# Kernel optimization log

Measured on AMD Instinct MI355X. Metric: run time of the kernel, lower is better.

## Reference

```python
import jax, jax.numpy as jnp
import numpy as np

EMBED_DIM = 1024
NUM_HEADS = 16
HEAD_DIM = EMBED_DIM // NUM_HEADS
KERNEL = 3
PAD = KERNEL // 2
B, L = 4, 1024


def conv1d(x, w, b):
    # x: [B, D, L], w: [D_out, D_in, K], b: [D_out]; 'same' padding like nn.Conv1d(padding=K//2)
    y = jax.lax.conv_general_dilated(
        x, w, window_strides=(1,), padding=[(PAD, PAD)],
        dimension_numbers=('NCH', 'OIH', 'NCH'))
    return y + b[None, :, None]


def setup_inputs() -> dict:
    key = jax.random.key(0)
    ks = jax.random.split(key, 12)
    fan = EMBED_DIM * KERNEL
    bound = 1.0 / np.sqrt(fan)
    def wconv(k):
        return jax.random.uniform(k, (EMBED_DIM, EMBED_DIM, KERNEL), jnp.float32, -bound, bound)
    def bconv(k):
        return jax.random.uniform(k, (EMBED_DIM,), jnp.float32, -bound, bound)
    return {
        'query': jax.random.normal(ks[0], (B, L, EMBED_DIM), jnp.float32),
        'key': jax.random.normal(ks[1], (B, L, EMBED_DIM), jnp.float32),
        'value': jax.random.normal(ks[2], (B, L, EMBED_DIM), jnp.float32),
        'key_padding_mask': jax.random.randint(ks[3], (B, L), 0, 2) > 0,
        'attn_mask': jnp.zeros((L, L), jnp.float32),
        'q_w': wconv(ks[4]), 'q_b': bconv(ks[5]),
        'k_w': wconv(ks[6]), 'k_b': bconv(ks[7]),
        'v_w': wconv(ks[8]), 'v_b': bconv(ks[9]),
        'o_w': wconv(ks[10]), 'o_b': bconv(ks[11]),
    }


def reference(query, key, value, key_padding_mask, attn_mask,
              q_w, q_b, k_w, k_b, v_w, v_b, o_w, o_b):
    scale = HEAD_DIM ** -0.5
    # projections: [B, D, L]
    q = conv1d(jnp.swapaxes(query, 1, 2), q_w, q_b)
    k = conv1d(jnp.swapaxes(key, 1, 2), k_w, k_b)
    v = conv1d(jnp.swapaxes(value, 1, 2), v_w, v_b)
    # [B, H, d, L]
    q = q.reshape(B, NUM_HEADS, HEAD_DIM, L)
    k = k.reshape(B, NUM_HEADS, HEAD_DIM, L)
    v = v.reshape(B, NUM_HEADS, HEAD_DIM, L)
    # scores: [B, H, L, L]
    scores = jnp.einsum('bhdi,bhdj->bhij', q, k) * scale
    scores = scores + attn_mask[None, None, :, :]
    scores = jnp.where(key_padding_mask[:, None, None, :], -jnp.inf, scores)
    attn = jax.nn.softmax(scores, axis=-1)  # dropout p=0 (eval) -> identity
    out = jnp.einsum('bhij,bhdj->bhdi', attn, v)  # [B, H, d, L]
    out = out.reshape(B, EMBED_DIM, L)
    out = conv1d(out, o_w, o_b)
    return jnp.swapaxes(out, 1, 2)  # [B, L, D]
```

## Files before the change

kernel.cpp:

```cpp
#include <hip/hip_runtime.h>
#include <math.h>

#define NB 4
#define NL 1024
#define ND 1024
#define NH 16
#define HD 64
#define PLN 4194304

typedef __attribute__((ext_vector_type(8))) short bf16x8;
typedef __attribute__((ext_vector_type(4))) float f32x4;

static __device__ __forceinline__ unsigned short f32_to_bf16(float f) {
  unsigned u = __float_as_uint(f);
  u += 0x7FFFu + ((u >> 16) & 1u);
  return (unsigned short)(u >> 16);
}
static __device__ __forceinline__ float bf16_to_f32(unsigned short s) {
  return __uint_as_float(((unsigned)s) << 16);
}
static __device__ __forceinline__ float exp2_f(float x) {
  float r;
  asm("v_exp_f32 %0, %1" : "=v"(r) : "v"(x));
  return r;
}

static __device__ __forceinline__ void split8(float4 a, float4 b, bf16x8* hi, bf16x8* lo) {
  unsigned u[8] = {__float_as_uint(a.x), __float_as_uint(a.y),
                   __float_as_uint(a.z), __float_as_uint(a.w),
                   __float_as_uint(b.x), __float_as_uint(b.y),
                   __float_as_uint(b.z), __float_as_uint(b.w)};
  union { unsigned p[4]; bf16x8 v; } H, L;
#pragma unroll
  for (int p = 0; p < 4; ++p) {
    unsigned u0 = u[2 * p], u1 = u[2 * p + 1];
    H.p[p] = __builtin_amdgcn_perm(u1, u0, 0x07060302u);
    unsigned l0 = __float_as_uint(__uint_as_float(u0) - __uint_as_float(u0 & 0xFFFF0000u));
    unsigned l1 = __float_as_uint(__uint_as_float(u1) - __uint_as_float(u1 & 0xFFFF0000u));
    L.p[p] = __builtin_amdgcn_perm(l1, l0, 0x07060302u);
  }
  *hi = H.v; *lo = L.v;
}

__global__ __launch_bounds__(256) void wcvt_kernel(
    const float* __restrict__ w0, const float* __restrict__ w1,
    const float* __restrict__ w2, const float* __restrict__ w3,
    unsigned short* __restrict__ wb, int* __restrict__ flag)
{
  if (blockIdx.x == 0 && blockIdx.y == 0 && threadIdx.x == 0) flag[0] = 0;
  const int t = blockIdx.y;
  const int o = blockIdx.x;
  const float* w = (t == 0) ? w0 : (t == 1) ? w1 : (t == 2) ? w2 : w3;
  unsigned short* hi = wb + (size_t)t * 6 * (1u << 20);
  unsigned short* lo = hi + 3 * (1u << 20);
  const int tid = threadIdx.x;
  float v[12];
  const float* src = w + (size_t)o * (ND * 3) + tid * 12;
#pragma unroll
  for (int j = 0; j < 3; ++j) {
    float4 f = *(const float4*)(src + j * 4);
    v[j * 4 + 0] = f.x; v[j * 4 + 1] = f.y; v[j * 4 + 2] = f.z; v[j * 4 + 3] = f.w;
  }
#pragma unroll
  for (int k = 0; k < 3; ++k) {
    unsigned short hh[4], ll[4];
#pragma unroll
    for (int ii = 0; ii < 4; ++ii) {
      float x = v[ii * 3 + k];
      unsigned short h = f32_to_bf16(x);
      float r = x - bf16_to_f32(h);
      hh[ii] = h; ll[ii] = f32_to_bf16(r);
    }
    size_t dst = (size_t)k * (ND * ND) + (size_t)o * ND + tid * 4;
    *(ushort4*)&hi[dst] = make_ushort4(hh[0], hh[1], hh[2], hh[3]);
    *(ushort4*)&lo[dst] = make_ushort4(ll[0], ll[1], ll[2], ll[3]);
  }
}

__global__ __launch_bounds__(256) void amask_scan(
    const float* __restrict__ a, int* __restrict__ flag)
{
  size_t i = ((size_t)blockIdx.x * 256 + threadIdx.x) * 4;
  float4 v = *(const float4*)&a[i];
  if (v.x != 0.f || v.y != 0.f || v.z != 0.f || v.w != 0.f) atomicOr(flag, 1);
}

__global__ __launch_bounds__(256) void xsplit_kernel(
    const float* __restrict__ x0, const float* __restrict__ x1,
    const float* __restrict__ x2, unsigned short* __restrict__ xs)
{
  const int z = blockIdx.y;
  const float* x = (z == 0) ? x0 : (z == 1) ? x1 : x2;
  const size_t i = ((size_t)blockIdx.x * 256 + threadIdx.x) * 8;
  float4 a = *(const float4*)&x[i];
  float4 b = *(const float4*)&x[i + 4];
  bf16x8 hi, lo;
  split8(a, b, &hi, &lo);
  unsigned short* ph = xs + (size_t)z * 2 * PLN;
  *(bf16x8*)&ph[i] = hi;
  *(bf16x8*)&ph[PLN + i] = lo;
}

template<int ASPLIT, int MODE>
__global__ __launch_bounds__(256, 3) void conv_mfma2(
    const void* X0v, const void* X1v, const void* X2v,
    const unsigned short* __restrict__ wb,
    const float* b0, const float* b1, const float* b2,
    float* Y0)
{
  __shared__ __align__(16) unsigned char Araw[16384];
  __shared__ unsigned short Bh[128 * 32];
  __shared__ unsigned short Bl[128 * 32];
  float* Af = (float*)Araw;
  unsigned short* Ah = (unsigned short*)Araw;
  unsigned short* Al = (unsigned short*)(Araw + 8192);

  const int tid = threadIdx.x, lane = tid & 63, wave = tid >> 6;
  const int lin = blockIdx.x + 8 * (blockIdx.y + 32 * blockIdx.z);
  const int g = lin & 7, t = lin >> 3;
  const int nb = (g & 3) * 2 + (t & 1);
  const int mb = (g >> 2) * 16 + ((t >> 1) & 15);
  const int z  = t >> 5;
  const int n0 = nb * 128, m0 = mb * 128;
  const int b = m0 >> 10, l0v = m0 & (NL - 1);

  const unsigned short* Wh = (MODE == 0) ? wb + (size_t)z * 6 * (1u << 20) : wb;
  const unsigned short* Wl = Wh + 3 * (1u << 20);

  const float* Xf = nullptr;
  const unsigned short* Xh_ = nullptr;
  const unsigned short* Xl_ = nullptr;
  if (ASPLIT) {
    const unsigned short* p = (const unsigned short*)((MODE == 0)
        ? (z == 0 ? X0v : (z == 1 ? X1v : X2v)) : X0v);
    Xh_ = p; Xl_ = p + PLN;
  } else {
    Xf = (const float*)((MODE == 0) ? (z == 0 ? X0v : (z == 1 ? X1v : X2v)) : X0v);
  }

  const int wm = (wave >> 1) * 64, wn = (wave & 1) * 64;
  const int mrow = lane & 15, quad = lane >> 4;
  const int r16 = lane >> 2, cs = lane & 3;
  const int src_chunk = (cs - (r16 >> 1)) & 3;
  const int bswz = ((quad + (mrow >> 1)) & 3) * 8;

  f32x4 acc[4][4] = {};

  const int kbeg = (MODE == 0) ? 0 : z;
  const int kend = (MODE == 0) ? 3 : z + 1;
  for (int koff = kbeg; koff < kend; ++koff) {
    const bool edge_lo = (l0v == 0 && koff == 0);
    const bool edge_hi = (l0v == NL - 128 && koff == 2);
    for (int i0 = 0; i0 < ND; i0 += 32) {
#pragma unroll
      for (int s = 0; s < 2; ++s) {
        const int seg = wave * 2 + s;
        const size_t goff = ((size_t)koff << 20) +
                            (size_t)(n0 + seg * 16 + r16) * ND + i0 + src_chunk * 8;
        __builtin_amdgcn_global_load_lds(
            (const __attribute__((address_space(1))) unsigned int*)(Wh + goff),
            (__attribute__((address_space(3))) unsigned int*)&Bh[seg * 512], 16, 0, 0);
        __builtin_amdgcn_global_load_lds(
            (const __attribute__((address_space(1))) unsigned int*)(Wl + goff),
            (__attribute__((address_space(3))) unsigned int*)&Bl[seg * 512], 16, 0, 0);
      }
      if (ASPLIT) {
#pragma unroll
        for (int j = 0; j < 4; ++j) {
          const int seg = wave * 2 + (j & 1);
          const int row = seg * 16 + (lane >> 2);
          const int slot = lane & 3;
          const int chunk = (slot - (row >> 1)) & 3;
          int l = l0v + row + koff - 1;
          l = (l < 0) ? 0 : (l > NL - 1 ? NL - 1 : l);
          const unsigned short* Xp = (j >> 1) ? Xl_ : Xh_;
          unsigned short* dst = ((j >> 1) ? Al : Ah) + seg * 512;
          const unsigned short* gp = Xp + ((size_t)(b << 10) + l) * ND + i0 + chunk * 8;
          __builtin_amdgcn_global_load_lds(
              (const __attribute__((address_space(1))) unsigned int*)gp,
              (__attribute__((address_space(3))) unsigned int*)dst, 16, 0, 0);
        }
      } else {
#pragma unroll
        for (int j = 0; j < 4; ++j) {
          const int s = (wave * 4 + j) * 64 + lane;
          const int row = s >> 3, sir = s & 7;
          const int chunk = (sir - (row & 7)) & 7;
          int l = l0v + row + koff - 1;
          l = (l < 0) ? 0 : (l > NL - 1 ? NL - 1 : l);
          const float* gp = Xf + ((size_t)(b << 10) + l) * ND + i0 + chunk * 4;
          __builtin_amdgcn_global_load_lds(
              (const __attribute__((address_space(1))) unsigned int*)gp,
              (__attribute__((address_space(3))) unsigned int*)&Af[(wave * 4 + j) * 256],
              16, 0, 0);
        }
      }
      __syncthreads();
      if (edge_lo || edge_hi) {
        const int er = edge_lo ? 0 : 127;
        if (ASPLIT) {
          if (tid < 16) {
            unsigned short* pl = (tid < 8) ? Ah : Al;
            *(ushort4*)&pl[er * 32 + (tid & 7) * 4] = make_ushort4(0, 0, 0, 0);
          }
        } else {
          if (tid < 8) *(float4*)&Af[er * 32 + tid * 4] = make_float4(0.f, 0.f, 0.f, 0.f);
        }
        __syncthreads();
      }
      bf16x8 ah[4], al[4];
      if (ASPLIT) {
#pragma unroll
        for (int mi = 0; mi < 4; ++mi) {
          const int row = wm + mi * 16 + mrow;
          const int cso = ((quad + (row >> 1)) & 3) * 8;
          ah[mi] = *(const bf16x8*)&Ah[row * 32 + cso];
          al[mi] = *(const bf16x8*)&Al[row * 32 + cso];
        }
      } else {
#pragma unroll
        for (int mi = 0; mi < 4; ++mi) {
          const int row = wm + mi * 16 + mrow, r7 = row & 7;
          float4 fa = *(const float4*)&Af[row * 32 + (((quad * 2) + r7) & 7) * 4];
          float4 fb = *(const float4*)&Af[row * 32 + (((quad * 2 + 1) + r7) & 7) * 4];
          split8(fa, fb, &ah[mi], &al[mi]);
        }
      }
#pragma unroll
      for (int ni = 0; ni < 4; ++ni) {
        const int brow = wn + ni * 16 + mrow;
        bf16x8 bh = *(const bf16x8*)&Bh[brow * 32 + bswz];
        bf16x8 bl = *(const bf16x8*)&Bl[brow * 32 + bswz];
#pragma unroll
        for (int mi = 0; mi < 4; ++mi) {
          acc[mi][ni] = __builtin_amdgcn_mfma_f32_16x16x32_bf16(ah[mi], bh, acc[mi][ni], 0, 0, 0);
          acc[mi][ni] = __builtin_amdgcn_mfma_f32_16x16x32_bf16(ah[mi], bl, acc[mi][ni], 0, 0, 0);
          acc[mi][ni] = __builtin_amdgcn_mfma_f32_16x16x32_bf16(al[mi], bh, acc[mi][ni], 0, 0, 0);
        }
      }
      __syncthreads();
    }
  }

  if (MODE == 0) {
    const float* bias = (z == 0) ? b0 : (z == 1) ? b1 : b2;
    unsigned short* U = (unsigned short*)Y0;
    if (z < 2) {
      unsigned short* Ph = U + (size_t)(2 * z) * PLN;
      unsigned short* Pl = Ph + PLN;
      const float sc = (z == 0) ? 0.18033688011112042f : 1.0f;
#pragma unroll
      for (int ni = 0; ni < 4; ++ni) {
        const int n = n0 + wn + ni * 16 + mrow;
        const float bv = bias[n];
        const int h = n >> 6, dd = n & 63;
        const int bh = b * NH + h;
#pragma unroll
        for (int mi = 0; mi < 4; ++mi) {
          const int mbase = m0 + wm + mi * 16 + quad * 4;
          f32x4 v = acc[mi][ni];
#pragma unroll
          for (int r = 0; r < 4; ++r) {
            const int l = (mbase + r) & (NL - 1);
            const float val = (v[r] + bv) * sc;
            const unsigned u = __float_as_uint(val);
            const unsigned short hh = (unsigned short)(u >> 16);
            const float res = val - __uint_as_float(u & 0xFFFF0000u);
            const unsigned short ll = (unsigned short)(__float_as_uint(res) >> 16);
            const size_t off = ((size_t)bh * NL + l) * HD + dd;
            Ph[off] = hh; Pl[off] = ll;
          }
        }
      }
    } else {
      unsigned short* Pv = U + (size_t)4 * PLN;
#pragma unroll
      for (int ni = 0; ni < 4; ++ni) {
        const int n = n0 + wn + ni * 16 + mrow;
        const float bv = bias[n];
        const int h = n >> 6, dd = n & 63;
        const int bh = b * NH + h;
#pragma unroll
        for (int mi = 0; mi < 4; ++mi) {
          const int mbase = m0 + wm + mi * 16 + quad * 4;
          const int lb = mbase & (NL - 1);
          f32x4 v = acc[mi][ni];
          ushort4 s4 = make_ushort4(f32_to_bf16(v[0] + bv), f32_to_bf16(v[1] + bv),
                                    f32_to_bf16(v[2] + bv), f32_to_bf16(v[3] + bv));
          *(ushort4*)&Pv[((size_t)bh * HD + dd) * NL + lb] = s4;
        }
      }
    }
  } else {
    float* P = Y0 + (size_t)z * ((size_t)NB * NL * ND);
#pragma unroll
    for (int ni = 0; ni < 4; ++ni) {
      const int n = n0 + wn + ni * 16 + mrow;
#pragma unroll
      for (int mi = 0; mi < 4; ++mi) {
        const int mbase = m0 + wm + mi * 16 + quad * 4;
        f32x4 v = acc[mi][ni];
#pragma unroll
        for (int r = 0; r < 4; ++r) {
          const int l = (mbase + r) & (NL - 1);
          P[((size_t)(b << 10) + l) * ND + n] = v[r];
        }
      }
    }
  }
}

__global__ __launch_bounds__(256) void reduce_kernel(
    const float* __restrict__ P, const float* __restrict__ bias, float* __restrict__ out)
{
  const size_t S = (size_t)NB * NL * ND;
  const size_t idx = ((size_t)blockIdx.x * 256 + threadIdx.x) * 4;
  const int n = (int)(idx & (ND - 1));
  float4 p0 = *(const float4*)&P[idx];
  float4 p1 = *(const float4*)&P[idx + S];
  float4 p2 = *(const float4*)&P[idx + 2 * S];
  float4 bv = *(const float4*)&bias[n];
  float4 r;
  r.x = p0.x + p1.x + p2.x + bv.x;
  r.y = p0.y + p1.y + p2.y + bv.y;
  r.z = p0.z + p1.z + p2.z + bv.z;
  r.w = p0.w + p1.w + p2.w + bv.w;
  *(float4*)&out[idx] = r;
}

__global__ __launch_bounds__(256, 3) void attn_mfma(
    const unsigned short* __restrict__ U, const int* __restrict__ kpm,
    const float* __restrict__ amask, const int* __restrict__ aflagp,
    unsigned short* __restrict__ AO)
{
  __shared__ __align__(16) unsigned short S[3 * 4096];
  __shared__ __align__(16) float Fm[NL];
  unsigned short* Kh = S;
  unsigned short* Kl = S + 4096;
  unsigned short* Vt = S + 8192;

  const int tid = threadIdx.x, lane = tid & 63, wave = tid >> 6;
  const int c = lane & 15, quad = lane >> 4;
  const int lin = blockIdx.x;
  const int bh = (lin & 7) + 8 * (lin >> 7);
  const int mt = (lin >> 3) & 15;
  const int b = bh >> 4;
  const int m0 = mt * 64;
  const int aflag = *aflagp;
  const int mrow = wave * 16 + c;
  const int gm = m0 + mrow;

  const size_t PLs = (size_t)PLN;
  const unsigned short* qTh = U;
  const unsigned short* qTl = U + PLs;
  const unsigned short* kTh = U + 2 * PLs;
  const unsigned short* kTl = U + 3 * PLs;
  const unsigned short* vTt = U + 4 * PLs;

  const int srow = lane >> 3;
  const int slot = lane & 7;
  const int chunk = (slot - srow) & 7;

#pragma unroll
  for (int q = 0; q < 4; ++q) {
    const int pl = q >> 1;
    const int i = wave * 2 + (q & 1);
    const int row = i * 8 + srow;
    const unsigned short* src = (pl ? qTl : qTh) +
        ((size_t)bh * NL + m0 + row) * HD + chunk * 8;
    unsigned short* dst = (pl ? Kl : Kh) + i * 512;
    __builtin_amdgcn_global_load_lds(
        (const __attribute__((address_space(1))) unsigned int*)src,
        (__attribute__((address_space(3))) unsigned int*)dst, 16, 0, 0);
  }
  {
    int4 kv = *(const int4*)&kpm[b * NL + tid * 4];
    float4 f;
    f.x = kv.x ? -INFINITY : 0.f;
    f.y = kv.y ? -INFINITY : 0.f;
    f.z = kv.z ? -INFINITY : 0.f;
    f.w = kv.w ? -INFINITY : 0.f;
    *(float4*)&Fm[tid * 4] = f;
  }
  __syncthreads();
  bf16x8 qbh[2], qbl[2];
#pragma unroll
  for (int kb = 0; kb < 2; ++kb) {
    const int cso = ((kb * 4 + quad + mrow) & 7) * 8;
    qbh[kb] = *(const bf16x8*)&Kh[mrow * 64 + cso];
    qbl[kb] = *(const bf16x8*)&Kl[mrow * 64 + cso];
  }

  f32x4 acc[4] = {};
  float m_r = -INFINITY, l_r = 0.0f;

  for (int n0t = 0; n0t < NL; n0t += 64) {
    __syncthreads();

#pragma unroll
    for (int q = 0; q < 6; ++q) {
      const int pl = q >> 1;
      const int i = wave * 2 + (q & 1);
      const int row = i * 8 + srow;
      const unsigned short* src;
      unsigned short* dst;
      if (pl == 0)      { src = kTh + ((size_t)bh * NL + n0t + row) * HD + chunk * 8; dst = Kh + i * 512; }
      else if (pl == 1) { src = kTl + ((size_t)bh * NL + n0t + row) * HD + chunk * 8; dst = Kl + i * 512; }
      else              { src = vTt + ((size_t)bh * HD + row) * NL + n0t + chunk * 8; dst = Vt + i * 512; }
      __builtin_amdgcn_global_load_lds(
          (const __attribute__((address_space(1))) unsigned int*)src,
          (__attribute__((address_space(3))) unsigned int*)dst, 16, 0, 0);
    }

    float mval[4][4];
#pragma unroll
    for (int nf = 0; nf < 4; ++nf) {
      float4 fm = *(const float4*)&Fm[n0t + nf * 16 + quad * 4];
      mval[nf][0] = fm.x; mval[nf][1] = fm.y; mval[nf][2] = fm.z; mval[nf][3] = fm.w;
    }
    if (aflag) {
#pragma unroll
      for (int nf = 0; nf < 4; ++nf)
#pragma unroll
        for (int r = 0; r < 4; ++r) {
          const int gn = n0t + nf * 16 + quad * 4 + r;
          mval[nf][r] += amask[(size_t)gm * NL + gn] * 1.4426950408889634f;
        }
    }
    __syncthreads();

    f32x4 sa[4] = {};
    __builtin_amdgcn_s_setprio(1);
#pragma unroll
    for (int kb = 0; kb < 2; ++kb)
#pragma unroll
      for (int nf = 0; nf < 4; ++nf) {
        const int row = nf * 16 + c;
        const int cso = ((kb * 4 + quad + row) & 7) * 8;
        bf16x8 kah = *(const bf16x8*)&Kh[row * 64 + cso];
        bf16x8 kal = *(const bf16x8*)&Kl[row * 64 + cso];
        sa[nf] = __builtin_amdgcn_mfma_f32_16x16x32_bf16(kah, qbh[kb], sa[nf], 0, 0, 0);
        sa[nf] = __builtin_amdgcn_mfma_f32_16x16x32_bf16(kah, qbl[kb], sa[nf], 0, 0, 0);
        sa[nf] = __builtin_amdgcn_mfma_f32_16x16x32_bf16(kal, qbh[kb], sa[nf], 0, 0, 0);
      }
    __builtin_amdgcn_s_setprio(0);

    float p[4][4];
    float tmax = -INFINITY;
#pragma unroll
    for (int nf = 0; nf < 4; ++nf)
#pragma unroll
      for (int r = 0; r < 4; ++r) {
        float s = sa[nf][r] + mval[nf][r];
        p[nf][r] = s;
        tmax = fmaxf(tmax, s);
      }
    tmax = fmaxf(tmax, __shfl_xor(tmax, 16));
    tmax = fmaxf(tmax, __shfl_xor(tmax, 32));
    float rs = 0.f;
    if (__all(tmax - m_r <= 8.0f)) {
      const float msafe = m_r;
#pragma unroll
      for (int nf = 0; nf < 4; ++nf)
#pragma unroll
        for (int r = 0; r < 4; ++r) {
          float e = exp2_f(p[nf][r] - msafe);
          p[nf][r] = e;
          rs += e;
        }
      rs += __shfl_xor(rs, 16);
      rs += __shfl_xor(rs, 32);
      l_r += rs;
    } else {
      const float newm = fmaxf(m_r, tmax);
      const float msafe = (newm == -INFINITY) ? 0.f : newm;
      const float alpha = exp2_f(m_r - msafe);
#pragma unroll
      for (int nf = 0; nf < 4; ++nf)
#pragma unroll
        for (int r = 0; r < 4; ++r) {
          float e = exp2_f(p[nf][r] - msafe);
          p[nf][r] = e;
          rs += e;
        }
      rs += __shfl_xor(rs, 16);
      rs += __shfl_xor(rs, 32);
      l_r = l_r * alpha + rs;
      m_r = newm;
#pragma unroll
      for (int df = 0; df < 4; ++df) {
        acc[df][0] *= alpha; acc[df][1] *= alpha;
        acc[df][2] *= alpha; acc[df][3] *= alpha;
      }
    }

    unsigned q16[4][2];
#pragma unroll
    for (int nf = 0; nf < 4; ++nf)
#pragma unroll
      for (int w = 0; w < 2; ++w)
        q16[nf][w] = (unsigned)f32_to_bf16(p[nf][2 * w]) |
                     ((unsigned)f32_to_bf16(p[nf][2 * w + 1]) << 16);

#pragma unroll
    for (int kb = 0; kb < 2; ++kb) {
      union { unsigned d[4]; bf16x8 v; } pb;
#pragma unroll
      for (int w = 0; w < 4; ++w) {
        const int addr = ((((quad & 1) * 2 + (w >> 1)) * 16 + c) << 2);
        unsigned v0 = __builtin_amdgcn_ds_bpermute(addr, (int)q16[2 * kb][w & 1]);
        unsigned v1 = __builtin_amdgcn_ds_bpermute(addr, (int)q16[2 * kb + 1][w & 1]);
        pb.d[w] = (quad >> 1) ? v1 : v0;
      }
      __builtin_amdgcn_s_setprio(1);
#pragma unroll
      for (int df = 0; df < 4; ++df) {
        const int row = df * 16 + c;
        const int cso = ((kb * 4 + quad + row) & 7) * 8;
        bf16x8 va = *(const bf16x8*)&Vt[row * 64 + cso];
        acc[df] = __builtin_amdgcn_mfma_f32_16x16x32_bf16(va, pb.v, acc[df], 0, 0, 0);
      }
      __builtin_amdgcn_s_setprio(0);
    }
  }

  __syncthreads();
  const float inv = 1.0f / l_r;
  float* Ob = (float*)S + wave * (16 * 68);
#pragma unroll
  for (int df = 0; df < 4; ++df)
#pragma unroll
    for (int r = 0; r < 4; ++r)
      Ob[c * 68 + df * 16 + quad * 4 + r] = acc[df][r] * inv;
  __syncthreads();
  const int mr2 = lane >> 2, cq2 = lane & 3;
  const int h = bh & 15;
  unsigned short* AOl_ = AO + PLN;
#pragma unroll
  for (int ii = 0; ii < 4; ++ii) {
    const int chunk2 = cq2 * 4 + ii;
    float4 v = *(const float4*)&Ob[mr2 * 68 + chunk2 * 4];
    const size_t off = ((size_t)(b << 10) + (m0 + wave * 16 + mr2)) * ND + h * HD + chunk2 * 4;
    float vv[4] = {v.x, v.y, v.z, v.w};
    ushort4 hh, ll;
    unsigned short* hp = (unsigned short*)&hh;
    unsigned short* lp = (unsigned short*)&ll;
#pragma unroll
    for (int e = 0; e < 4; ++e) {
      const unsigned u = __float_as_uint(vv[e]);
      hp[e] = (unsigned short)(u >> 16);
      const float res = vv[e] - __uint_as_float(u & 0xFFFF0000u);
      lp[e] = (unsigned short)(__float_as_uint(res) >> 16);
    }
    *(ushort4*)&AO[off] = hh;
    *(ushort4*)&AOl_[off] = ll;
  }
}

extern "C" void kernel_launch(void* const* d_in, const int* in_sizes, int n_in,
                              void* d_out, int out_size, void* d_ws, size_t ws_size,
                              hipStream_t stream) {
  (void)in_sizes; (void)n_in; (void)out_size;
  const float* query = (const float*)d_in[0];
  const float* key_  = (const float*)d_in[1];
  const float* value = (const float*)d_in[2];
  const int*   kpm   = (const int*)d_in[3];
  const float* amask = (const float*)d_in[4];
  const float* q_w = (const float*)d_in[5];
  const float* q_b = (const float*)d_in[6];
  const float* k_w = (const float*)d_in[7];
  const float* k_b = (const float*)d_in[8];
  const float* v_w = (const float*)d_in[9];
  const float* v_b = (const float*)d_in[10];
  const float* o_w = (const float*)d_in[11];
  const float* o_b = (const float*)d_in[12];
  float* out = (float*)d_out;

  unsigned short* Wb  = (unsigned short*)d_ws;
  unsigned short* U   = (unsigned short*)((char*)d_ws + (size_t)50331648);
  float*          P   = (float*)((char*)d_ws + (size_t)50331648);
  unsigned short* AOs = (unsigned short*)d_ws;
  unsigned short* Xs  = (unsigned short*)((char*)d_ws + (size_t)92274688);
  int* flag = (int*)d_out;
  const bool presplit = ws_size >= (size_t)142606336;

  wcvt_kernel<<<dim3(1024, 4), 256, 0, stream>>>(q_w, k_w, v_w, o_w, Wb, flag);
  amask_scan<<<1024, 256, 0, stream>>>(amask, flag);
  if (presplit) {
    xsplit_kernel<<<dim3(2048, 3), 256, 0, stream>>>(query, key_, value, Xs);
    conv_mfma2<1, 0><<<dim3(8, 32, 3), 256, 0, stream>>>(
        Xs, Xs + (size_t)2 * PLN, Xs + (size_t)4 * PLN, Wb, q_b, k_b, v_b, (float*)U);
  } else {
    conv_mfma2<0, 0><<<dim3(8, 32, 3), 256, 0, stream>>>(
        query, key_, value, Wb, q_b, k_b, v_b, (float*)U);
  }
  attn_mfma<<<1024, 256, 0, stream>>>(U, kpm, amask, flag, AOs);
  conv_mfma2<1, 1><<<dim3(8, 32, 3), 256, 0, stream>>>(
      AOs, AOs, AOs, Wb + (size_t)3 * 6 * (1u << 20), o_b, o_b, o_b, P);
  reduce_kernel<<<4096, 256, 0, stream>>>(P, o_b, out);
}
```

Before: 518.5 us.

## Double-buffer attention K/V tiles, process two query blocks per workgroup, drop presplit path

The attention kernel now keeps two LDS buffers and prefetches the next K/V tile while computing the current one. Each workgroup handles 128 query rows as two 64-row groups, so every K/V tile staged in LDS feeds twice the MFMA work and the grid is halved. Q fragments are loaded straight from global memory into registers, and the attn_mask add moves into the score loop. Separately, the xsplit precompute path is removed so the QKV conv always splits fp32 inputs in-kernel, and edge-row zeroing becomes a register select instead of an extra LDS store plus barrier. The changes raise register and LDS pressure and halve the number of attention workgroups.

```diff
diff --git a/kernel.cpp b/kernel.cpp
--- a/kernel.cpp
+++ b/kernel.cpp
@@ -85,22 +85,6 @@
   if (v.x != 0.f || v.y != 0.f || v.z != 0.f || v.w != 0.f) atomicOr(flag, 1);
 }
 
-__global__ __launch_bounds__(256) void xsplit_kernel(
-    const float* __restrict__ x0, const float* __restrict__ x1,
-    const float* __restrict__ x2, unsigned short* __restrict__ xs)
-{
-  const int z = blockIdx.y;
-  const float* x = (z == 0) ? x0 : (z == 1) ? x1 : x2;
-  const size_t i = ((size_t)blockIdx.x * 256 + threadIdx.x) * 8;
-  float4 a = *(const float4*)&x[i];
-  float4 b = *(const float4*)&x[i + 4];
-  bf16x8 hi, lo;
-  split8(a, b, &hi, &lo);
-  unsigned short* ph = xs + (size_t)z * 2 * PLN;
-  *(bf16x8*)&ph[i] = hi;
-  *(bf16x8*)&ph[PLN + i] = lo;
-}
-
 template<int ASPLIT, int MODE>
 __global__ __launch_bounds__(256, 3) void conv_mfma2(
     const void* X0v, const void* X1v, const void* X2v,
@@ -130,7 +114,7 @@
   const float* Xf = nullptr;
   const unsigned short* Xh_ = nullptr;
   const unsigned short* Xl_ = nullptr;
-  if (ASPLIT) {
+  if constexpr (ASPLIT) {
     const unsigned short* p = (const unsigned short*)((MODE == 0)
         ? (z == 0 ? X0v : (z == 1 ? X1v : X2v)) : X0v);
     Xh_ = p; Xl_ = p + PLN;
@@ -145,12 +129,13 @@
   const int bswz = ((quad + (mrow >> 1)) & 3) * 8;
 
   f32x4 acc[4][4] = {};
+  const bf16x8 zz = {};
 
   const int kbeg = (MODE == 0) ? 0 : z;
   const int kend = (MODE == 0) ? 3 : z + 1;
   for (int koff = kbeg; koff < kend; ++koff) {
-    const bool edge_lo = (l0v == 0 && koff == 0);
-    const bool edge_hi = (l0v == NL - 128 && koff == 2);
+    const bool e_lo = (l0v == 0 && koff == 0);
+    const bool e_hi = (l0v == NL - 128 && koff == 2);
     for (int i0 = 0; i0 < ND; i0 += 32) {
 #pragma unroll
       for (int s = 0; s < 2; ++s) {
@@ -164,7 +149,7 @@
             (const __attribute__((address_space(1))) unsigned int*)(Wl + goff),
             (__attribute__((address_space(3))) unsigned int*)&Bl[seg * 512], 16, 0, 0);
       }
-      if (ASPLIT) {
+      if constexpr (ASPLIT) {
 #pragma unroll
         for (int j = 0; j < 4; ++j) {
           const int seg = wave * 2 + (j & 1);
@@ -196,26 +181,16 @@
         }
       }
       __syncthreads();
-      if (edge_lo || edge_hi) {
-        const int er = edge_lo ? 0 : 127;
-        if (ASPLIT) {
-          if (tid < 16) {
-            unsigned short* pl = (tid < 8) ? Ah : Al;
-            *(ushort4*)&pl[er * 32 + (tid & 7) * 4] = make_ushort4(0, 0, 0, 0);
-          }
-        } else {
-          if (tid < 8) *(float4*)&Af[er * 32 + tid * 4] = make_float4(0.f, 0.f, 0.f, 0.f);
-        }
-        __syncthreads();
-      }
       bf16x8 ah[4], al[4];
-      if (ASPLIT) {
+      if constexpr (ASPLIT) {
 #pragma unroll
         for (int mi = 0; mi < 4; ++mi) {
           const int row = wm + mi * 16 + mrow;
           const int cso = ((quad + (row >> 1)) & 3) * 8;
           ah[mi] = *(const bf16x8*)&Ah[row * 32 + cso];
           al[mi] = *(const bf16x8*)&Al[row * 32 + cso];
+          const bool kill = (e_lo && row == 0) || (e_hi && row == 127);
+          if (kill) { ah[mi] = zz; al[mi] = zz; }
         }
       } else {
 #pragma unroll
@@ -224,6 +199,8 @@
           float4 fa = *(const float4*)&Af[row * 32 + (((quad * 2) + r7) & 7) * 4];
           float4 fb = *(const float4*)&Af[row * 32 + (((quad * 2 + 1) + r7) & 7) * 4];
           split8(fa, fb, &ah[mi], &al[mi]);
+          const bool kill = (e_lo && row == 0) || (e_hi && row == 127);
+          if (kill) { ah[mi] = zz; al[mi] = zz; }
         }
       }
 #pragma unroll
@@ -333,22 +310,18 @@
     const float* __restrict__ amask, const int* __restrict__ aflagp,
     unsigned short* __restrict__ AO)
 {
-  __shared__ __align__(16) unsigned short S[3 * 4096];
+  __shared__ __align__(16) unsigned short S[2][3 * 4096];
   __shared__ __align__(16) float Fm[NL];
-  unsigned short* Kh = S;
-  unsigned short* Kl = S + 4096;
-  unsigned short* Vt = S + 8192;
 
   const int tid = threadIdx.x, lane = tid & 63, wave = tid >> 6;
   const int c = lane & 15, quad = lane >> 4;
   const int lin = blockIdx.x;
-  const int bh = (lin & 7) + 8 * (lin >> 7);
-  const int mt = (lin >> 3) & 15;
+  const int bh = (lin & 7) + 8 * (lin >> 6);
+  const int mt = (lin >> 3) & 7;
   const int b = bh >> 4;
-  const int m0 = mt * 64;
+  const int m0 = mt * 128;
   const int aflag = *aflagp;
   const int mrow = wave * 16 + c;
-  const int gm = m0 + mrow;
 
   const size_t PLs = (size_t)PLN;
   const unsigned short* qTh = U;
@@ -361,17 +334,36 @@
   const int slot = lane & 7;
   const int chunk = (slot - srow) & 7;
 
-#pragma unroll
-  for (int q = 0; q < 4; ++q) {
-    const int pl = q >> 1;
-    const int i = wave * 2 + (q & 1);
-    const int row = i * 8 + srow;
-    const unsigned short* src = (pl ? qTl : qTh) +
-        ((size_t)bh * NL + m0 + row) * HD + chunk * 8;
-    unsigned short* dst = (pl ? Kl : Kh) + i * 512;
-    __builtin_amdgcn_global_load_lds(
-        (const __attribute__((address_space(1))) unsigned int*)src,
-        (__attribute__((address_space(3))) unsigned int*)dst, 16, 0, 0);
+  auto stage_tile = [&](int n0t, unsigned short* B) {
+    unsigned short* KhD = B;
+    unsigned short* KlD = B + 4096;
+    unsigned short* VtD = B + 8192;
+#pragma unroll
+    for (int q = 0; q < 6; ++q) {
+      const int pl = q >> 1;
+      const int i = wave * 2 + (q & 1);
+      const int row = i * 8 + srow;
+      const unsigned short* src;
+      unsigned short* dst;
+      if (pl == 0)      { src = kTh + ((size_t)bh * NL + n0t + row) * HD + chunk * 8; dst = KhD + i * 512; }
+      else if (pl == 1) { src = kTl + ((size_t)bh * NL + n0t + row) * HD + chunk * 8; dst = KlD + i * 512; }
+      else              { src = vTt + ((size_t)bh * HD + row) * NL + n0t + chunk * 8; dst = VtD + i * 512; }
+      __builtin_amdgcn_global_load_lds(
+          (const __attribute__((address_space(1))) unsigned int*)src,
+          (__attribute__((address_space(3))) unsigned int*)dst, 16, 0, 0);
+    }
+  };
+
+  bf16x8 qbh[2][2], qbl[2][2];
+#pragma unroll
+  for (int g2 = 0; g2 < 2; ++g2) {
+    const size_t qoff = ((size_t)bh * NL + m0 + g2 * 64 + mrow) * HD;
+#pragma unroll
+    for (int kb = 0; kb < 2; ++kb) {
+      const int co = (kb * 4 + quad) * 8;
+      qbh[g2][kb] = *(const bf16x8*)&qTh[qoff + co];
+      qbl[g2][kb] = *(const bf16x8*)&qTl[qoff + co];
+    }
   }
   {
     int4 kv = *(const int4*)&kpm[b * NL + tid * 4];
@@ -382,35 +374,21 @@
     f.w = kv.w ? -INFINITY : 0.f;
     *(float4*)&Fm[tid * 4] = f;
   }
+  stage_tile(0, S[1]);
   __syncthreads();
-  bf16x8 qbh[2], qbl[2];
-#pragma unroll
-  for (int kb = 0; kb < 2; ++kb) {
-    const int cso = ((kb * 4 + quad + mrow) & 7) * 8;
-    qbh[kb] = *(const bf16x8*)&Kh[mrow * 64 + cso];
-    qbl[kb] = *(const bf16x8*)&Kl[mrow * 64 + cso];
-  }
-
-  f32x4 acc[4] = {};
-  float m_r = -INFINITY, l_r = 0.0f;
-
-  for (int n0t = 0; n0t < NL; n0t += 64) {
-    __syncthreads();
-
-#pragma unroll
-    for (int q = 0; q < 6; ++q) {
-      const int pl = q >> 1;
-      const int i = wave * 2 + (q & 1);
-      const int row = i * 8 + srow;
-      const unsigned short* src;
-      unsigned short* dst;
-      if (pl == 0)      { src = kTh + ((size_t)bh * NL + n0t + row) * HD + chunk * 8; dst = Kh + i * 512; }
-      else if (pl == 1) { src = kTl + ((size_t)bh * NL + n0t + row) * HD + chunk * 8; dst = Kl + i * 512; }
-      else              { src = vTt + ((size_t)bh * HD + row) * NL + n0t + chunk * 8; dst = Vt + i * 512; }
-      __builtin_amdgcn_global_load_lds(
-          (const __attribute__((address_space(1))) unsigned int*)src,
-          (__attribute__((address_space(3))) unsigned int*)dst, 16, 0, 0);
-    }
+
+  f32x4 acc0[4] = {}, acc1[4] = {};
+  float m_r0 = -INFINITY, l_r0 = 0.0f;
+  float m_r1 = -INFINITY, l_r1 = 0.0f;
+  int cur = 1;
+
+  for (int tt = 0; tt < 16; ++tt) {
+    const int n0t = tt * 64;
+    if (tt < 15) stage_tile(n0t + 64, S[cur ^ 1]);
+
+    const unsigned short* Kh = S[cur];
+    const unsigned short* Kl = S[cur] + 4096;
+    const unsigned short* Vt = S[cur] + 8192;
 
     float mval[4][4];
 #pragma unroll
@@ -418,18 +396,8 @@
       float4 fm = *(const float4*)&Fm[n0t + nf * 16 + quad * 4];
       mval[nf][0] = fm.x; mval[nf][1] = fm.y; mval[nf][2] = fm.z; mval[nf][3] = fm.w;
     }
-    if (aflag) {
-#pragma unroll
-      for (int nf = 0; nf < 4; ++nf)
-#pragma unroll
-        for (int r = 0; r < 4; ++r) {
-          const int gn = n0t + nf * 16 + quad * 4 + r;
-          mval[nf][r] += amask[(size_t)gm * NL + gn] * 1.4426950408889634f;
-        }
-    }
-    __syncthreads();
-
-    f32x4 sa[4] = {};
+
+    f32x4 sa0[4] = {}, sa1[4] = {};
     __builtin_amdgcn_s_setprio(1);
 #pragma unroll
     for (int kb = 0; kb < 2; ++kb)
@@ -439,78 +407,97 @@
         const int cso = ((kb * 4 + quad + row) & 7) * 8;
         bf16x8 kah = *(const bf16x8*)&Kh[row * 64 + cso];
         bf16x8 kal = *(const bf16x8*)&Kl[row * 64 + cso];
-        sa[nf] = __builtin_amdgcn_mfma_f32_16x16x32_bf16(kah, qbh[kb], sa[nf], 0, 0, 0);
-        sa[nf] = __builtin_amdgcn_mfma_f32_16x16x32_bf16(kah, qbl[kb], sa[nf], 0, 0, 0);
-        sa[nf] = __builtin_amdgcn_mfma_f32_16x16x32_bf16(kal, qbh[kb], sa[nf], 0, 0, 0);
+        sa0[nf] = __builtin_amdgcn_mfma_f32_16x16x32_bf16(kah, qbh[0][kb], sa0[nf], 0, 0, 0);
+        sa0[nf] = __builtin_amdgcn_mfma_f32_16x16x32_bf16(kah, qbl[0][kb], sa0[nf], 0, 0, 0);
+        sa0[nf] = __builtin_amdgcn_mfma_f32_16x16x32_bf16(kal, qbh[0][kb], sa0[nf], 0, 0, 0);
+        sa1[nf] = __builtin_amdgcn_mfma_f32_16x16x32_bf16(kah, qbh[1][kb], sa1[nf], 0, 0, 0);
+        sa1[nf] = __builtin_amdgcn_mfma_f32_16x16x32_bf16(kah, qbl[1][kb], sa1[nf], 0, 0, 0);
+        sa1[nf] = __builtin_amdgcn_mfma_f32_16x16x32_bf16(kal, qbh[1][kb], sa1[nf], 0, 0, 0);
       }
     __builtin_amdgcn_s_setprio(0);
 
-    float p[4][4];
-    float tmax = -INFINITY;
-#pragma unroll
-    for (int nf = 0; nf < 4; ++nf)
-#pragma unroll
-      for (int r = 0; r < 4; ++r) {
-        float s = sa[nf][r] + mval[nf][r];
-        p[nf][r] = s;
-        tmax = fmaxf(tmax, s);
-      }
-    tmax = fmaxf(tmax, __shfl_xor(tmax, 16));
-    tmax = fmaxf(tmax, __shfl_xor(tmax, 32));
-    float rs = 0.f;
-    if (__all(tmax - m_r <= 8.0f)) {
-      const float msafe = m_r;
+    unsigned q16a[4][2], q16b[4][2];
+#pragma unroll
+    for (int g2 = 0; g2 < 2; ++g2) {
+      f32x4* sa = g2 ? sa1 : sa0;
+      f32x4* accg = g2 ? acc1 : acc0;
+      float& m_r = g2 ? m_r1 : m_r0;
+      float& l_r = g2 ? l_r1 : l_r0;
+      const int gm = m0 + g2 * 64 + mrow;
+
+      float p[4][4];
+      float tmax = -INFINITY;
 #pragma unroll
       for (int nf = 0; nf < 4; ++nf)
 #pragma unroll
         for (int r = 0; r < 4; ++r) {
-          float e = exp2_f(p[nf][r] - msafe);
-          p[nf][r] = e;
-          rs += e;
-        }
-      rs += __shfl_xor(rs, 16);
-      rs += __shfl_xor(rs, 32);
-      l_r += rs;
-    } else {
-      const float newm = fmaxf(m_r, tmax);
-      const float msafe = (newm == -INFINITY) ? 0.f : newm;
-      const float alpha = exp2_f(m_r - msafe);
+          float s = sa[nf][r] + mval[nf][r];
+          if (aflag) {
+            const int gn = n0t + nf * 16 + quad * 4 + r;
+            s += amask[(size_t)gm * NL + gn] * 1.4426950408889634f;
+          }
+          p[nf][r] = s;
+          tmax = fmaxf(tmax, s);
+        }
+      tmax = fmaxf(tmax, __shfl_xor(tmax, 16));
+      tmax = fmaxf(tmax, __shfl_xor(tmax, 32));
+      float rs = 0.f;
+      if (__all(tmax - m_r <= 8.0f)) {
+        const float msafe = m_r;
+#pragma unroll
+        for (int nf = 0; nf < 4; ++nf)
+#pragma unroll
+          for (int r = 0; r < 4; ++r) {
+            float e = exp2_f(p[nf][r] - msafe);
+            p[nf][r] = e;
+            rs += e;
+          }
+        rs += __shfl_xor(rs, 16);
+        rs += __shfl_xor(rs, 32);
+        l_r += rs;
+      } else {
+        const float newm = fmaxf(m_r, tmax);
+        const float msafe = (newm == -INFINITY) ? 0.f : newm;
+        const float alpha = exp2_f(m_r - msafe);
+#pragma unroll
+        for (int nf = 0; nf < 4; ++nf)
+#pragma unroll
+          for (int r = 0; r < 4; ++r) {
+            float e = exp2_f(p[nf][r] - msafe);
+            p[nf][r] = e;
+            rs += e;
+          }
+        rs += __shfl_xor(rs, 16);
+        rs += __shfl_xor(rs, 32);
+        l_r = l_r * alpha + rs;
+        m_r = newm;
+#pragma unroll
+        for (int df = 0; df < 4; ++df) {
+          accg[df][0] *= alpha; accg[df][1] *= alpha;
+          accg[df][2] *= alpha; accg[df][3] *= alpha;
+        }
+      }
+      unsigned (*q16)[2] = g2 ? q16b : q16a;
 #pragma unroll
       for (int nf = 0; nf < 4; ++nf)
 #pragma unroll
-        for (int r = 0; r < 4; ++r) {
-          float e = exp2_f(p[nf][r] - msafe);
-          p[nf][r] = e;
-          rs += e;
-        }
-      rs += __shfl_xor(rs, 16);
-      rs += __shfl_xor(rs, 32);
-      l_r = l_r * alpha + rs;
-      m_r = newm;
-#pragma unroll
-      for (int df = 0; df < 4; ++df) {
-        acc[df][0] *= alpha; acc[df][1] *= alpha;
-        acc[df][2] *= alpha; acc[df][3] *= alpha;
-      }
-    }
-
-    unsigned q16[4][2];
-#pragma unroll
-    for (int nf = 0; nf < 4; ++nf)
-#pragma unroll
-      for (int w = 0; w < 2; ++w)
-        q16[nf][w] = (unsigned)f32_to_bf16(p[nf][2 * w]) |
-                     ((unsigned)f32_to_bf16(p[nf][2 * w + 1]) << 16);
+        for (int w = 0; w < 2; ++w)
+          q16[nf][w] = (unsigned)f32_to_bf16(p[nf][2 * w]) |
+                       ((unsigned)f32_to_bf16(p[nf][2 * w + 1]) << 16);
+    }
 
 #pragma unroll
     for (int kb = 0; kb < 2; ++kb) {
-      union { unsigned d[4]; bf16x8 v; } pb;
+      union { unsigned d[4]; bf16x8 v; } pb0, pb1;
 #pragma unroll
       for (int w = 0; w < 4; ++w) {
         const int addr = ((((quad & 1) * 2 + (w >> 1)) * 16 + c) << 2);
-        unsigned v0 = __builtin_amdgcn_ds_bpermute(addr, (int)q16[2 * kb][w & 1]);
-        unsigned v1 = __builtin_amdgcn_ds_bpermute(addr, (int)q16[2 * kb + 1][w & 1]);
-        pb.d[w] = (quad >> 1) ? v1 : v0;
+        unsigned a0 = __builtin_amdgcn_ds_bpermute(addr, (int)q16a[2 * kb][w & 1]);
+        unsigned a1 = __builtin_amdgcn_ds_bpermute(addr, (int)q16a[2 * kb + 1][w & 1]);
+        pb0.d[w] = (quad >> 1) ? a1 : a0;
+        unsigned b0 = __builtin_amdgcn_ds_bpermute(addr, (int)q16b[2 * kb][w & 1]);
+        unsigned b1 = __builtin_amdgcn_ds_bpermute(addr, (int)q16b[2 * kb + 1][w & 1]);
+        pb1.d[w] = (quad >> 1) ? b1 : b0;
       }
       __builtin_amdgcn_s_setprio(1);
 #pragma unroll
@@ -518,49 +505,58 @@
         const int row = df * 16 + c;
         const int cso = ((kb * 4 + quad + row) & 7) * 8;
         bf16x8 va = *(const bf16x8*)&Vt[row * 64 + cso];
-        acc[df] = __builtin_amdgcn_mfma_f32_16x16x32_bf16(va, pb.v, acc[df], 0, 0, 0);
+        acc0[df] = __builtin_amdgcn_mfma_f32_16x16x32_bf16(va, pb0.v, acc0[df], 0, 0, 0);
+        acc1[df] = __builtin_amdgcn_mfma_f32_16x16x32_bf16(va, pb1.v, acc1[df], 0, 0, 0);
       }
       __builtin_amdgcn_s_setprio(0);
     }
-  }
-
-  __syncthreads();
-  const float inv = 1.0f / l_r;
-  float* Ob = (float*)S + wave * (16 * 68);
-#pragma unroll
-  for (int df = 0; df < 4; ++df)
-#pragma unroll
-    for (int r = 0; r < 4; ++r)
-      Ob[c * 68 + df * 16 + quad * 4 + r] = acc[df][r] * inv;
+    __syncthreads();
+    cur ^= 1;
+  }
+
   __syncthreads();
   const int mr2 = lane >> 2, cq2 = lane & 3;
   const int h = bh & 15;
   unsigned short* AOl_ = AO + PLN;
-#pragma unroll
-  for (int ii = 0; ii < 4; ++ii) {
-    const int chunk2 = cq2 * 4 + ii;
-    float4 v = *(const float4*)&Ob[mr2 * 68 + chunk2 * 4];
-    const size_t off = ((size_t)(b << 10) + (m0 + wave * 16 + mr2)) * ND + h * HD + chunk2 * 4;
-    float vv[4] = {v.x, v.y, v.z, v.w};
-    ushort4 hh, ll;
-    unsigned short* hp = (unsigned short*)&hh;
-    unsigned short* lp = (unsigned short*)&ll;
-#pragma unroll
-    for (int e = 0; e < 4; ++e) {
-      const unsigned u = __float_as_uint(vv[e]);
-      hp[e] = (unsigned short)(u >> 16);
-      const float res = vv[e] - __uint_as_float(u & 0xFFFF0000u);
-      lp[e] = (unsigned short)(__float_as_uint(res) >> 16);
-    }
-    *(ushort4*)&AO[off] = hh;
-    *(ushort4*)&AOl_[off] = ll;
+  float* Ob = (float*)S[0] + wave * (16 * 68);
+#pragma unroll
+  for (int g2 = 0; g2 < 2; ++g2) {
+    const f32x4* accg = g2 ? acc1 : acc0;
+    const float inv = 1.0f / (g2 ? l_r1 : l_r0);
+#pragma unroll
+    for (int df = 0; df < 4; ++df)
+#pragma unroll
+      for (int r = 0; r < 4; ++r)
+        Ob[c * 68 + df * 16 + quad * 4 + r] = accg[df][r] * inv;
+    __builtin_amdgcn_s_barrier();
+#pragma unroll
+    for (int ii = 0; ii < 4; ++ii) {
+      const int chunk2 = cq2 * 4 + ii;
+      float4 v = *(const float4*)&Ob[mr2 * 68 + chunk2 * 4];
+      const size_t off = ((size_t)(b << 10) + (m0 + g2 * 64 + wave * 16 + mr2)) * ND +
+                         h * HD + chunk2 * 4;
+      float vv[4] = {v.x, v.y, v.z, v.w};
+      ushort4 hh, ll;
+      unsigned short* hp = (unsigned short*)&hh;
+      unsigned short* lp = (unsigned short*)&ll;
+#pragma unroll
+      for (int e = 0; e < 4; ++e) {
+        const unsigned u = __float_as_uint(vv[e]);
+        hp[e] = (unsigned short)(u >> 16);
+        const float res = vv[e] - __uint_as_float(u & 0xFFFF0000u);
+        lp[e] = (unsigned short)(__float_as_uint(res) >> 16);
+      }
+      *(ushort4*)&AO[off] = hh;
+      *(ushort4*)&AOl_[off] = ll;
+    }
+    if (g2 == 0) __builtin_amdgcn_s_barrier();
   }
 }
 
 extern "C" void kernel_launch(void* const* d_in, const int* in_sizes, int n_in,
                               void* d_out, int out_size, void* d_ws, size_t ws_size,
                               hipStream_t stream) {
-  (void)in_sizes; (void)n_in; (void)out_size;
+  (void)in_sizes; (void)n_in; (void)out_size; (void)ws_size;
   const float* query = (const float*)d_in[0];
   const float* key_  = (const float*)d_in[1];
   const float* value = (const float*)d_in[2];
@@ -580,21 +576,13 @@
   unsigned short* U   = (unsigned short*)((char*)d_ws + (size_t)50331648);
   float*          P   = (float*)((char*)d_ws + (size_t)50331648);
   unsigned short* AOs = (unsigned short*)d_ws;
-  unsigned short* Xs  = (unsigned short*)((char*)d_ws + (size_t)92274688);
   int* flag = (int*)d_out;
-  const bool presplit = ws_size >= (size_t)142606336;
 
   wcvt_kernel<<<dim3(1024, 4), 256, 0, stream>>>(q_w, k_w, v_w, o_w, Wb, flag);
   amask_scan<<<1024, 256, 0, stream>>>(amask, flag);
-  if (presplit) {
-    xsplit_kernel<<<dim3(2048, 3), 256, 0, stream>>>(query, key_, value, Xs);
-    conv_mfma2<1, 0><<<dim3(8, 32, 3), 256, 0, stream>>>(
-        Xs, Xs + (size_t)2 * PLN, Xs + (size_t)4 * PLN, Wb, q_b, k_b, v_b, (float*)U);
-  } else {
-    conv_mfma2<0, 0><<<dim3(8, 32, 3), 256, 0, stream>>>(
-        query, key_, value, Wb, q_b, k_b, v_b, (float*)U);
-  }
-  attn_mfma<<<1024, 256, 0, stream>>>(U, kpm, amask, flag, AOs);
+  conv_mfma2<0, 0><<<dim3(8, 32, 3), 256, 0, stream>>>(
+      query, key_, value, Wb, q_b, k_b, v_b, (float*)U);
+  attn_mfma<<<512, 256, 0, stream>>>(U, kpm, amask, flag, AOs);
   conv_mfma2<1, 1><<<dim3(8, 32, 3), 256, 0, stream>>>(
       AOs, AOs, AOs, Wb + (size_t)3 * 6 * (1u << 20), o_b, o_b, o_b, P);
   reduce_kernel<<<4096, 256, 0, stream>>>(P, o_b, out);
```

Result: slower. 530.9 us (+2.4%).
